# Kernel optimization log

Hardware: AMD Instinct MI355X
Metric: run time of the kernel (lower is better)

## Reference

```python
import jax, jax.numpy as jnp
import numpy as np

D = 512   # dense write dimension
M = 64    # number of experts
B = 16    # per-expert sparse code width
N = 8192  # tokens
K = 4     # experts per token (top-k)


def _normalize_U(U):
    # UnitColNormPadded(dim=1): each column of the (D+1, b) expert matrix
    # is rescaled to unit L2 norm along the padded (D+1) axis.
    nrm = jnp.sqrt(jnp.sum(U * U, axis=1, keepdims=True))
    return U / nrm


def setup_inputs() -> dict:
    key = jax.random.key(0)
    k1, k2, k3 = jax.random.split(key, 3)
    h_sparse = jax.random.normal(k1, (N, K, B), dtype=jnp.float32)
    topk_idxs = jax.random.randint(k2, (N, K), 0, M)
    U = jax.random.normal(k3, (M, D + 1, B), dtype=jnp.float32)
    return {"h_sparse": h_sparse, "topk_idxs": topk_idxs, "U": U}


def reference(h_sparse, topk_idxs, U):
    Un = _normalize_U(U)                      # (m, D+1, b)
    U_active = Un[topk_idxs][:, :, :D, :]     # gather -> (N, k, D, b)
    writes = jnp.einsum('nkdb,nkb->nd', U_active, h_sparse)   # (N, D)
    h_recon = jnp.einsum('nkdb,nd->nkb', U_active, writes)    # (N, k, b)
    h_target = jax.lax.stop_gradient(h_sparse)
    diff = h_recon - h_target
    writer_aux_loss = jnp.mean(diff * diff)
    return writes, writer_aux_loss
```

## Files before the change

kernel.cpp:

```cpp
#include <hip/hip_runtime.h>

#define DD 512
#define MM 64
#define BB 16
#define NN 8192
#define KK 4
#define DP1 513
#define CAP 1024
#define NPAIR (NN * KK)

#define CNT_B  0
#define BKT_B  33024
#define U_B    164096
#define UT_B   1212672
#define WBF_B  2261248
#define PART_B 10649856
#define WS_NEED 44204288

typedef unsigned int uint;
typedef unsigned short ushort;
typedef __attribute__((ext_vector_type(8))) short short8;
typedef __attribute__((ext_vector_type(4))) float f32x4;

__device__ __forceinline__ ushort f2bf(float f) {
    uint u = __builtin_bit_cast(uint, f);
    uint r = (u + 0x7FFFu + ((u >> 16) & 1u)) >> 16;
    return (ushort)r;
}
__device__ __forceinline__ float bf2f(ushort s) {
    return __builtin_bit_cast(float, (uint)s << 16);
}

__global__ __launch_bounds__(256) void prep_build(
    const float* __restrict__ U,
    const int*   __restrict__ topk,
    void* __restrict__ ws,
    float* __restrict__ loss_slot)
{
    const int blk = blockIdx.x, t = threadIdx.x;

    if (blk < 256) {
        const int m = blk >> 2, sl = blk & 3;
        const float* Um = U + (long)m * DP1 * BB;

        __shared__ float red[256];
        __shared__ float inv_s[BB];
        __shared__ ushort tr[BB][136];

        float a = 0.f;
        for (int i = t; i < DP1 * BB; i += 256) { float v = Um[i]; a += v * v; }
        red[t] = a;
        __syncthreads();
        if (t < BB) {
            float tot = 0.f;
            #pragma unroll
            for (int j = 0; j < 16; ++j) tot += red[t + 16 * j];
            inv_s[t] = rsqrtf(tot);
        }
        __syncthreads();

        ushort* ub = (ushort*)((char*)ws + U_B) + (long)m * DD * BB + sl * 2048;
        ushort* ut = (ushort*)((char*)ws + UT_B) + (long)m * BB * DD + sl * 128;
        const float* Us = Um + sl * 2048;

        #pragma unroll
        for (int iter = 0; iter < 4; ++iter) {
            const int i = t + iter * 256;
            const int e0 = 2 * i;
            const int dl = e0 >> 4, b0 = e0 & 15;
            const float2 v = *(const float2*)(Us + e0);
            const ushort bv0 = f2bf(v.x * inv_s[b0]);
            const ushort bv1 = f2bf(v.y * inv_s[b0 + 1]);
            *(uint*)(ub + e0) = (uint)bv0 | ((uint)bv1 << 16);
            tr[b0][dl]     = bv0;
            tr[b0 + 1][dl] = bv1;
        }
        __syncthreads();
        {
            const int b = t >> 4, doff = (t & 15) * 8;
            uint4 val;
            val.x = (uint)tr[b][doff + 0] | ((uint)tr[b][doff + 1] << 16);
            val.y = (uint)tr[b][doff + 2] | ((uint)tr[b][doff + 3] << 16);
            val.z = (uint)tr[b][doff + 4] | ((uint)tr[b][doff + 5] << 16);
            val.w = (uint)tr[b][doff + 6] | ((uint)tr[b][doff + 7] << 16);
            *(uint4*)(ut + (long)b * DD + doff) = val;
        }
    } else {
        const int cblk = blk - 256;
        int* cnt = (int*)ws;
        ushort* bkt = (ushort*)((char*)ws + BKT_B);
        __shared__ int lc[MM], lb[MM];
        if (t < MM) lc[t] = 0;
        __syncthreads();
        const int p = cblk * 256 + t;
        const int e = topk[p];
        const int my = atomicAdd(&lc[e], 1);
        __syncthreads();
        if (t < MM) lb[t] = atomicAdd(&cnt[t], lc[t]);
        __syncthreads();
        bkt[e * CAP + lb[e] + my] = (ushort)p;
        if (cblk == 0 && t == 0) *loss_slot = 0.f;
    }
}

__global__ __launch_bounds__(256) void pass_writes_mfma(
    const float* __restrict__ h_sparse, void* __restrict__ ws)
{
    const int e = blockIdx.x & 63, g = blockIdx.x >> 6;
    const int wave = threadIdx.x >> 6, lane = threadIdx.x & 63;
    const int quad = lane >> 4, l15 = lane & 15;

    const int* cnt = (const int*)ws;
    const ushort* bkt = (const ushort*)((const char*)ws + BKT_B);
    const ushort* Ue = (const ushort*)((const char*)ws + U_B) + (long)e * DD * BB;
    ushort* part = (ushort*)((char*)ws + PART_B);

    const int c  = cnt[e];
    const int lo = (c * g) >> 3;
    const int hi = (c * (g + 1)) >> 3;

    for (int base = lo + wave * 16; base < hi; base += 64) {
        const int pidx = base + l15;
        const bool valid = pidx < hi;
        const int id = valid ? (int)bkt[e * CAP + pidx] : 0;
        const int n = id >> 2, k = id & 3;

        short8 bfrag = (short8)0;
        if (quad < 2 && valid) {
            const float4* hp = (const float4*)(h_sparse + (long)id * BB + quad * 8);
            const float4 h0 = hp[0], h1 = hp[1];
            bfrag[0] = (short)f2bf(h0.x); bfrag[1] = (short)f2bf(h0.y);
            bfrag[2] = (short)f2bf(h0.z); bfrag[3] = (short)f2bf(h0.w);
            bfrag[4] = (short)f2bf(h1.x); bfrag[5] = (short)f2bf(h1.y);
            bfrag[6] = (short)f2bf(h1.z); bfrag[7] = (short)f2bf(h1.w);
        }
        ushort* prow = part + ((long)(k * NN + n) << 9);

        #pragma unroll 2
        for (int dt = 0; dt < 32; dt += 2) {
            short8 a0 = (short8)0, a1 = (short8)0;
            if (quad < 2) {
                a0 = *(const short8*)(Ue + ((long)(dt * 16 + l15) << 4) + quad * 8);
                a1 = *(const short8*)(Ue + ((long)((dt + 1) * 16 + l15) << 4) + quad * 8);
            }
            f32x4 z = {0.f, 0.f, 0.f, 0.f};
            f32x4 c0 = __builtin_amdgcn_mfma_f32_16x16x32_bf16(a0, bfrag, z, 0, 0, 0);
            f32x4 c1 = __builtin_amdgcn_mfma_f32_16x16x32_bf16(a1, bfrag, z, 0, 0, 0);

            uint p0x = (uint)f2bf(c0[0]) | ((uint)f2bf(c0[1]) << 16);
            uint p0y = (uint)f2bf(c0[2]) | ((uint)f2bf(c0[3]) << 16);
            uint p1x = (uint)f2bf(c1[0]) | ((uint)f2bf(c1[1]) << 16);
            uint p1y = (uint)f2bf(c1[2]) | ((uint)f2bf(c1[3]) << 16);
            uint q0x = __shfl_xor((int)p0x, 16, 64);
            uint q0y = __shfl_xor((int)p0y, 16, 64);
            uint q1x = __shfl_xor((int)p1x, 16, 64);
            uint q1y = __shfl_xor((int)p1y, 16, 64);

            if (valid) {
                uint4 st;
                int sdt;
                if ((quad & 1) == 0) { st.x = p0x; st.y = p0y; st.z = q0x; st.w = q0y; sdt = dt; }
                else                 { st.x = q1x; st.y = q1y; st.z = p1x; st.w = p1y; sdt = dt + 1; }
                const int srow = (quad & 2) ? 8 : 0;
                *(uint4*)(prow + sdt * 16 + srow) = st;
            }
        }
    }
}

__global__ __launch_bounds__(256) void reduce_w(
    void* __restrict__ ws, float* __restrict__ out)
{
    const uint4* part4 = (const uint4*)((const char*)ws + PART_B);
    uint4* wbf4 = (uint4*)((char*)ws + WBF_B);
    const int gsz = NN * DD / 8;
    const int gid = blockIdx.x * 256 + threadIdx.x;

    const uint4 v0 = part4[gid];
    const uint4 v1 = part4[(long)gsz + gid];
    const uint4 v2 = part4[2L * gsz + gid];
    const uint4 v3 = part4[3L * gsz + gid];

    float s[8];
    s[0] = bf2f((ushort)v0.x) + bf2f((ushort)v1.x) + bf2f((ushort)v2.x) + bf2f((ushort)v3.x);
    s[1] = bf2f((ushort)(v0.x >> 16)) + bf2f((ushort)(v1.x >> 16)) + bf2f((ushort)(v2.x >> 16)) + bf2f((ushort)(v3.x >> 16));
    s[2] = bf2f((ushort)v0.y) + bf2f((ushort)v1.y) + bf2f((ushort)v2.y) + bf2f((ushort)v3.y);
    s[3] = bf2f((ushort)(v0.y >> 16)) + bf2f((ushort)(v1.y >> 16)) + bf2f((ushort)(v2.y >> 16)) + bf2f((ushort)(v3.y >> 16));
    s[4] = bf2f((ushort)v0.z) + bf2f((ushort)v1.z) + bf2f((ushort)v2.z) + bf2f((ushort)v3.z);
    s[5] = bf2f((ushort)(v0.z >> 16)) + bf2f((ushort)(v1.z >> 16)) + bf2f((ushort)(v2.z >> 16)) + bf2f((ushort)(v3.z >> 16));
    s[6] = bf2f((ushort)v0.w) + bf2f((ushort)v1.w) + bf2f((ushort)v2.w) + bf2f((ushort)v3.w);
    s[7] = bf2f((ushort)(v0.w >> 16)) + bf2f((ushort)(v1.w >> 16)) + bf2f((ushort)(v2.w >> 16)) + bf2f((ushort)(v3.w >> 16));

    float4* out4 = (float4*)out;
    out4[(long)gid * 2 + 0] = make_float4(s[0], s[1], s[2], s[3]);
    out4[(long)gid * 2 + 1] = make_float4(s[4], s[5], s[6], s[7]);

    uint4 pk;
    pk.x = (uint)f2bf(s[0]) | ((uint)f2bf(s[1]) << 16);
    pk.y = (uint)f2bf(s[2]) | ((uint)f2bf(s[3]) << 16);
    pk.z = (uint)f2bf(s[4]) | ((uint)f2bf(s[5]) << 16);
    pk.w = (uint)f2bf(s[6]) | ((uint)f2bf(s[7]) << 16);
    wbf4[gid] = pk;
}

__global__ __launch_bounds__(256) void pass_recon_mfma(
    const float* __restrict__ h_sparse, void* __restrict__ ws,
    float* __restrict__ out)
{
    const int e = blockIdx.x & 63, g = blockIdx.x >> 6;
    const int wave = threadIdx.x >> 6, lane = threadIdx.x & 63;
    const int quad = lane >> 4, l15 = lane & 15;
    const int t = threadIdx.x;

    const int* cnt = (const int*)ws;
    const ushort* bkt = (const ushort*)((const char*)ws + BKT_B);
    const ushort* Ute = (const ushort*)((const char*)ws + UT_B) + (long)e * BB * DD;
    const ushort* wbf = (const ushort*)((const char*)ws + WBF_B);

    __shared__ float loss_blk;
    if (t == 0) loss_blk = 0.f;
    __syncthreads();

    const int c  = cnt[e];
    const int lo = (c * g) >> 3;
    const int hi = (c * (g + 1)) >> 3;

    float lsum = 0.f;
    for (int base = lo + wave * 16; base < hi; base += 64) {
        const int pidx = base + l15;
        const bool valid = pidx < hi;
        const int id = valid ? (int)bkt[e * CAP + pidx] : 0;
        const int n = id >> 2;
        const ushort* wrow = wbf + ((long)n << 9);

        f32x4 acc = {0.f, 0.f, 0.f, 0.f};
        #pragma unroll 4
        for (int kk = 0; kk < 16; ++kk) {
            const int doff = kk * 32 + quad * 8;
            const short8 afrag = *(const short8*)(wrow + doff);
            const short8 bfrag = *(const short8*)(Ute + (long)l15 * DD + doff);
            acc = __builtin_amdgcn_mfma_f32_16x16x32_bf16(afrag, bfrag, acc, 0, 0, 0);
        }
        #pragma unroll
        for (int r = 0; r < 4; ++r) {
            const int pr = base + quad * 4 + r;
            if (pr < hi) {
                const int id2 = (int)bkt[e * CAP + pr];
                const float h = h_sparse[(long)id2 * BB + l15];
                const float d = acc[r] - h;
                lsum += d * d;
            }
        }
    }
    #pragma unroll
    for (int off = 32; off > 0; off >>= 1) lsum += __shfl_xor(lsum, off, 64);
    if (lane == 0 && lsum != 0.f) atomicAdd(&loss_blk, lsum);
    __syncthreads();
    if (t == 0 && loss_blk != 0.f)
        atomicAdd(out + (long)NN * DD, loss_blk * (1.0f / ((float)NN * KK * BB)));
}

__global__ __launch_bounds__(256) void norm_kernel(
    const float* __restrict__ U, float* __restrict__ inv_norm,
    float* __restrict__ loss_slot)
{
    const int m = blockIdx.x;
    const int t = threadIdx.x;
    const float* Um = U + (long)m * DP1 * BB;
    float acc = 0.f;
    for (int idx = t; idx < DP1 * BB; idx += 256) {
        float v = Um[idx];
        acc += v * v;
    }
    __shared__ float s[256];
    s[t] = acc;
    __syncthreads();
    if (t < BB) {
        float tot = 0.f;
        #pragma unroll
        for (int j = 0; j < 16; ++j) tot += s[t + 16 * j];
        inv_norm[m * BB + t] = rsqrtf(tot);
    }
    if (m == 0 && t == 0) *loss_slot = 0.f;
}

__global__ __launch_bounds__(256) void dense_write_kernel(
    const float* __restrict__ h_sparse,
    const int*   __restrict__ topk,
    const float* __restrict__ U,
    const float* __restrict__ inv_norm,
    float* __restrict__ out)
{
    const int n = blockIdx.x;
    const int t = threadIdx.x;

    __shared__ float hs[KK * BB];
    __shared__ float ho[KK * BB];
    __shared__ float inv_s[KK * BB];
    __shared__ int   eidx[KK];
    __shared__ float w_s[DD];
    __shared__ float red[256];

    if (t < KK) eidx[t] = topk[n * KK + t];
    __syncthreads();
    if (t < KK * BB) {
        const int k = t / BB, b = t % BB;
        const float h  = h_sparse[(long)n * KK * BB + t];
        const float iv = inv_norm[eidx[k] * BB + b];
        ho[t]    = h;
        inv_s[t] = iv;
        hs[t]    = h * iv;
    }
    __syncthreads();

    #pragma unroll
    for (int dd = 0; dd < 2; ++dd) {
        const int d = t + dd * 256;
        float w = 0.f;
        #pragma unroll
        for (int k = 0; k < KK; ++k) {
            const float4* row = (const float4*)(U + ((long)eidx[k] * DP1 + d) * BB);
            #pragma unroll
            for (int q = 0; q < 4; ++q) {
                const float4 u4 = row[q];
                w += u4.x * hs[k * BB + 4 * q + 0];
                w += u4.y * hs[k * BB + 4 * q + 1];
                w += u4.z * hs[k * BB + 4 * q + 2];
                w += u4.w * hs[k * BB + 4 * q + 3];
            }
        }
        w_s[d] = w;
        out[(long)n * DD + d] = w;
    }
    __syncthreads();

    {
        const int pair = t & 63;
        const int k = pair >> 4, b = pair & 15;
        const int ch = t >> 6;
        const float* Ucol = U + (long)eidx[k] * DP1 * BB + b;
        float p = 0.f;
        #pragma unroll 8
        for (int d = ch * 128; d < ch * 128 + 128; ++d) {
            p += Ucol[(long)d * BB] * w_s[d];
        }
        red[t] = p;
    }
    __syncthreads();

    if (t < 64) {
        const float recon = (red[t] + red[t + 64] + red[t + 128] + red[t + 192]) * inv_s[t];
        const float diff  = recon - ho[t];
        float sq = diff * diff;
        #pragma unroll
        for (int off = 32; off > 0; off >>= 1) sq += __shfl_down(sq, off, 64);
        if (t == 0) {
            atomicAdd(out + (long)NN * DD, sq * (1.0f / ((float)NN * KK * BB)));
        }
    }
}


extern "C" void kernel_launch(void* const* d_in, const int* in_sizes, int n_in,
                              void* d_out, int out_size, void* d_ws, size_t ws_size,
                              hipStream_t stream) {
    const float* h_sparse = (const float*)d_in[0];
    const int*   topk     = (const int*)d_in[1];
    const float* U        = (const float*)d_in[2];
    float* out = (float*)d_out;

    if (ws_size >= (size_t)WS_NEED) {
        hipMemsetAsync(d_ws, 0, 256, stream);
        hipLaunchKernelGGL(prep_build, dim3(256 + NPAIR / 256), dim3(256), 0, stream,
                           U, topk, d_ws, out + (long)NN * DD);
        hipLaunchKernelGGL(pass_writes_mfma, dim3(MM * 8), dim3(256), 0, stream,
                           h_sparse, d_ws);
        hipLaunchKernelGGL(reduce_w, dim3(NN * DD / 8 / 256), dim3(256), 0, stream,
                           d_ws, out);
        hipLaunchKernelGGL(pass_recon_mfma, dim3(MM * 8), dim3(256), 0, stream,
                           h_sparse, d_ws, out);
    } else {
        float* inv_norm = (float*)d_ws;
        hipLaunchKernelGGL(norm_kernel, dim3(MM), dim3(256), 0, stream,
                           U, inv_norm, out + (long)NN * DD);
        hipLaunchKernelGGL(dense_write_kernel, dim3(NN), dim3(256), 0, stream,
                           h_sparse, topk, U, inv_norm, out);
    }
}
```

Measured before the change: 126.5 us.

## Accumulate writes with fp32 atomics into output instead of partials plus reduce

Removes the per-k bf16 partial buffer and the separate reduce kernel. The writes pass now atomically adds MFMA results straight into a zeroed fp32 output, and the recon pass reads fp32 writes and converts them to bf16 on the fly. This saves a 32MB partial write-and-read round trip and one launch. In exchange it issues many scalar float atomics, adds a memset of the output, and makes the summation order nondeterministic.

```diff
diff --git a/kernel.cpp b/kernel.cpp
--- a/kernel.cpp
+++ b/kernel.cpp
@@ -10,12 +10,10 @@
 #define NPAIR (NN * KK)
 
 #define CNT_B  0
-#define BKT_B  33024
-#define U_B    164096
-#define UT_B   1212672
-#define WBF_B  2261248
-#define PART_B 10649856
-#define WS_NEED 44204288
+#define BKT_B  256
+#define U_B    131328
+#define UT_B   1179904
+#define WS_NEED 2228480
 
 typedef unsigned int uint;
 typedef unsigned short ushort;
@@ -34,8 +32,7 @@
 __global__ __launch_bounds__(256) void prep_build(
     const float* __restrict__ U,
     const int*   __restrict__ topk,
-    void* __restrict__ ws,
-    float* __restrict__ loss_slot)
+    void* __restrict__ ws)
 {
     const int blk = blockIdx.x, t = threadIdx.x;
 
@@ -99,12 +96,12 @@
         if (t < MM) lb[t] = atomicAdd(&cnt[t], lc[t]);
         __syncthreads();
         bkt[e * CAP + lb[e] + my] = (ushort)p;
-        if (cblk == 0 && t == 0) *loss_slot = 0.f;
-    }
-}
-
-__global__ __launch_bounds__(256) void pass_writes_mfma(
-    const float* __restrict__ h_sparse, void* __restrict__ ws)
+    }
+}
+
+__global__ __launch_bounds__(256) void pass_writes_at(
+    const float* __restrict__ h_sparse, const void* __restrict__ ws,
+    float* __restrict__ out)
 {
     const int e = blockIdx.x & 63, g = blockIdx.x >> 6;
     const int wave = threadIdx.x >> 6, lane = threadIdx.x & 63;
@@ -113,7 +110,6 @@
     const int* cnt = (const int*)ws;
     const ushort* bkt = (const ushort*)((const char*)ws + BKT_B);
     const ushort* Ue = (const ushort*)((const char*)ws + U_B) + (long)e * DD * BB;
-    ushort* part = (ushort*)((char*)ws + PART_B);
 
     const int c  = cnt[e];
     const int lo = (c * g) >> 3;
@@ -123,7 +119,7 @@
         const int pidx = base + l15;
         const bool valid = pidx < hi;
         const int id = valid ? (int)bkt[e * CAP + pidx] : 0;
-        const int n = id >> 2, k = id & 3;
+        const int n = id >> 2;
 
         short8 bfrag = (short8)0;
         if (quad < 2 && valid) {
@@ -134,77 +130,28 @@
             bfrag[4] = (short)f2bf(h1.x); bfrag[5] = (short)f2bf(h1.y);
             bfrag[6] = (short)f2bf(h1.z); bfrag[7] = (short)f2bf(h1.w);
         }
-        ushort* prow = part + ((long)(k * NN + n) << 9);
-
-        #pragma unroll 2
-        for (int dt = 0; dt < 32; dt += 2) {
-            short8 a0 = (short8)0, a1 = (short8)0;
-            if (quad < 2) {
-                a0 = *(const short8*)(Ue + ((long)(dt * 16 + l15) << 4) + quad * 8);
-                a1 = *(const short8*)(Ue + ((long)((dt + 1) * 16 + l15) << 4) + quad * 8);
+        float* orow = out + (long)n * DD;
+
+        #pragma unroll 4
+        for (int dt = 0; dt < 32; ++dt) {
+            short8 afrag = (short8)0;
+            if (quad < 2)
+                afrag = *(const short8*)(Ue + ((long)(dt * 16 + l15) << 4) + quad * 8);
+            f32x4 z = {0.f, 0.f, 0.f, 0.f};
+            f32x4 acc = __builtin_amdgcn_mfma_f32_16x16x32_bf16(afrag, bfrag, z, 0, 0, 0);
+            if (valid) {
+                float* p = orow + dt * 16 + quad * 4;
+                atomicAdd(p + 0, acc[0]);
+                atomicAdd(p + 1, acc[1]);
+                atomicAdd(p + 2, acc[2]);
+                atomicAdd(p + 3, acc[3]);
             }
-            f32x4 z = {0.f, 0.f, 0.f, 0.f};
-            f32x4 c0 = __builtin_amdgcn_mfma_f32_16x16x32_bf16(a0, bfrag, z, 0, 0, 0);
-            f32x4 c1 = __builtin_amdgcn_mfma_f32_16x16x32_bf16(a1, bfrag, z, 0, 0, 0);
-
-            uint p0x = (uint)f2bf(c0[0]) | ((uint)f2bf(c0[1]) << 16);
-            uint p0y = (uint)f2bf(c0[2]) | ((uint)f2bf(c0[3]) << 16);
-            uint p1x = (uint)f2bf(c1[0]) | ((uint)f2bf(c1[1]) << 16);
-            uint p1y = (uint)f2bf(c1[2]) | ((uint)f2bf(c1[3]) << 16);
-            uint q0x = __shfl_xor((int)p0x, 16, 64);
-            uint q0y = __shfl_xor((int)p0y, 16, 64);
-            uint q1x = __shfl_xor((int)p1x, 16, 64);
-            uint q1y = __shfl_xor((int)p1y, 16, 64);
-
-            if (valid) {
-                uint4 st;
-                int sdt;
-                if ((quad & 1) == 0) { st.x = p0x; st.y = p0y; st.z = q0x; st.w = q0y; sdt = dt; }
-                else                 { st.x = q1x; st.y = q1y; st.z = p1x; st.w = p1y; sdt = dt + 1; }
-                const int srow = (quad & 2) ? 8 : 0;
-                *(uint4*)(prow + sdt * 16 + srow) = st;
-            }
-        }
-    }
-}
-
-__global__ __launch_bounds__(256) void reduce_w(
-    void* __restrict__ ws, float* __restrict__ out)
-{
-    const uint4* part4 = (const uint4*)((const char*)ws + PART_B);
-    uint4* wbf4 = (uint4*)((char*)ws + WBF_B);
-    const int gsz = NN * DD / 8;
-    const int gid = blockIdx.x * 256 + threadIdx.x;
-
-    const uint4 v0 = part4[gid];
-    const uint4 v1 = part4[(long)gsz + gid];
-    const uint4 v2 = part4[2L * gsz + gid];
-    const uint4 v3 = part4[3L * gsz + gid];
-
-    float s[8];
-    s[0] = bf2f((ushort)v0.x) + bf2f((ushort)v1.x) + bf2f((ushort)v2.x) + bf2f((ushort)v3.x);
-    s[1] = bf2f((ushort)(v0.x >> 16)) + bf2f((ushort)(v1.x >> 16)) + bf2f((ushort)(v2.x >> 16)) + bf2f((ushort)(v3.x >> 16));
-    s[2] = bf2f((ushort)v0.y) + bf2f((ushort)v1.y) + bf2f((ushort)v2.y) + bf2f((ushort)v3.y);
-    s[3] = bf2f((ushort)(v0.y >> 16)) + bf2f((ushort)(v1.y >> 16)) + bf2f((ushort)(v2.y >> 16)) + bf2f((ushort)(v3.y >> 16));
-    s[4] = bf2f((ushort)v0.z) + bf2f((ushort)v1.z) + bf2f((ushort)v2.z) + bf2f((ushort)v3.z);
-    s[5] = bf2f((ushort)(v0.z >> 16)) + bf2f((ushort)(v1.z >> 16)) + bf2f((ushort)(v2.z >> 16)) + bf2f((ushort)(v3.z >> 16));
-    s[6] = bf2f((ushort)v0.w) + bf2f((ushort)v1.w) + bf2f((ushort)v2.w) + bf2f((ushort)v3.w);
-    s[7] = bf2f((ushort)(v0.w >> 16)) + bf2f((ushort)(v1.w >> 16)) + bf2f((ushort)(v2.w >> 16)) + bf2f((ushort)(v3.w >> 16));
-
-    float4* out4 = (float4*)out;
-    out4[(long)gid * 2 + 0] = make_float4(s[0], s[1], s[2], s[3]);
-    out4[(long)gid * 2 + 1] = make_float4(s[4], s[5], s[6], s[7]);
-
-    uint4 pk;
-    pk.x = (uint)f2bf(s[0]) | ((uint)f2bf(s[1]) << 16);
-    pk.y = (uint)f2bf(s[2]) | ((uint)f2bf(s[3]) << 16);
-    pk.z = (uint)f2bf(s[4]) | ((uint)f2bf(s[5]) << 16);
-    pk.w = (uint)f2bf(s[6]) | ((uint)f2bf(s[7]) << 16);
-    wbf4[gid] = pk;
-}
-
-__global__ __launch_bounds__(256) void pass_recon_mfma(
-    const float* __restrict__ h_sparse, void* __restrict__ ws,
+        }
+    }
+}
+
+__global__ __launch_bounds__(256) void pass_recon_f32(
+    const float* __restrict__ h_sparse, const void* __restrict__ ws,
     float* __restrict__ out)
 {
     const int e = blockIdx.x & 63, g = blockIdx.x >> 6;
@@ -215,7 +162,6 @@
     const int* cnt = (const int*)ws;
     const ushort* bkt = (const ushort*)((const char*)ws + BKT_B);
     const ushort* Ute = (const ushort*)((const char*)ws + UT_B) + (long)e * BB * DD;
-    const ushort* wbf = (const ushort*)((const char*)ws + WBF_B);
 
     __shared__ float loss_blk;
     if (t == 0) loss_blk = 0.f;
@@ -231,13 +177,19 @@
         const bool valid = pidx < hi;
         const int id = valid ? (int)bkt[e * CAP + pidx] : 0;
         const int n = id >> 2;
-        const ushort* wrow = wbf + ((long)n << 9);
+        const float* wrow = out + (long)n * DD;
 
         f32x4 acc = {0.f, 0.f, 0.f, 0.f};
         #pragma unroll 4
         for (int kk = 0; kk < 16; ++kk) {
             const int doff = kk * 32 + quad * 8;
-            const short8 afrag = *(const short8*)(wrow + doff);
+            const float4 f0 = *(const float4*)(wrow + doff);
+            const float4 f1 = *(const float4*)(wrow + doff + 4);
+            short8 afrag;
+            afrag[0] = (short)f2bf(f0.x); afrag[1] = (short)f2bf(f0.y);
+            afrag[2] = (short)f2bf(f0.z); afrag[3] = (short)f2bf(f0.w);
+            afrag[4] = (short)f2bf(f1.x); afrag[5] = (short)f2bf(f1.y);
+            afrag[6] = (short)f2bf(f1.z); afrag[7] = (short)f2bf(f1.w);
             const short8 bfrag = *(const short8*)(Ute + (long)l15 * DD + doff);
             acc = __builtin_amdgcn_mfma_f32_16x16x32_bf16(afrag, bfrag, acc, 0, 0, 0);
         }
@@ -371,13 +323,12 @@
 
     if (ws_size >= (size_t)WS_NEED) {
         hipMemsetAsync(d_ws, 0, 256, stream);
+        hipMemsetAsync(d_out, 0, ((size_t)NN * DD + 1) * 4, stream);
         hipLaunchKernelGGL(prep_build, dim3(256 + NPAIR / 256), dim3(256), 0, stream,
-                           U, topk, d_ws, out + (long)NN * DD);
-        hipLaunchKernelGGL(pass_writes_mfma, dim3(MM * 8), dim3(256), 0, stream,
-                           h_sparse, d_ws);
-        hipLaunchKernelGGL(reduce_w, dim3(NN * DD / 8 / 256), dim3(256), 0, stream,
-                           d_ws, out);
-        hipLaunchKernelGGL(pass_recon_mfma, dim3(MM * 8), dim3(256), 0, stream,
+                           U, topk, d_ws);
+        hipLaunchKernelGGL(pass_writes_at, dim3(MM * 8), dim3(256), 0, stream,
+                           h_sparse, d_ws, out);
+        hipLaunchKernelGGL(pass_recon_f32, dim3(MM * 8), dim3(256), 0, stream,
                            h_sparse, d_ws, out);
     } else {
         float* inv_norm = (float*)d_ws;
```

Result: slower. 347.8 us (+174.9%).

## Compute reconstruction loss via expert Gram matrices instead of re-reading writes

Applied to the files above, without the earlier changes.

Replaces the per-pair reconstruction pass (which re-read bf16 writes through a gather) with a precomputed 64x64 table of 16x16 expert Gram blocks U_e^T U_e'. The loss is then evaluated per token from h_sparse and the Gram blocks. The Gram computation is folded into the writes kernel's grid, and the loss is folded into the reduce kernel's grid. This removes one launch and the bf16 writes buffer round trip, at the cost of an extra 4 MB Gram table and somewhat different rounding, since the Gram path uses bf16 U and fp32 h.

```diff
diff --git a/kernel.cpp b/kernel.cpp
--- a/kernel.cpp
+++ b/kernel.cpp
@@ -10,12 +10,12 @@
 #define NPAIR (NN * KK)
 
 #define CNT_B  0
-#define BKT_B  33024
-#define U_B    164096
-#define UT_B   1212672
-#define WBF_B  2261248
-#define PART_B 10649856
-#define WS_NEED 44204288
+#define BKT_B  256
+#define U_B    131328
+#define UT_B   1179904
+#define G_B    2228480
+#define PART_B 6422784
+#define WS_NEED 39977216
 
 typedef unsigned int uint;
 typedef unsigned short ushort;
@@ -103,161 +103,158 @@
     }
 }
 
-__global__ __launch_bounds__(256) void pass_writes_mfma(
+__global__ __launch_bounds__(256) void writes_gram(
     const float* __restrict__ h_sparse, void* __restrict__ ws)
 {
-    const int e = blockIdx.x & 63, g = blockIdx.x >> 6;
-    const int wave = threadIdx.x >> 6, lane = threadIdx.x & 63;
+    const int blk = blockIdx.x, t = threadIdx.x;
+    const int wave = t >> 6, lane = t & 63;
     const int quad = lane >> 4, l15 = lane & 15;
 
-    const int* cnt = (const int*)ws;
-    const ushort* bkt = (const ushort*)((const char*)ws + BKT_B);
-    const ushort* Ue = (const ushort*)((const char*)ws + U_B) + (long)e * DD * BB;
-    ushort* part = (ushort*)((char*)ws + PART_B);
-
-    const int c  = cnt[e];
-    const int lo = (c * g) >> 3;
-    const int hi = (c * (g + 1)) >> 3;
-
-    for (int base = lo + wave * 16; base < hi; base += 64) {
-        const int pidx = base + l15;
-        const bool valid = pidx < hi;
-        const int id = valid ? (int)bkt[e * CAP + pidx] : 0;
-        const int n = id >> 2, k = id & 3;
-
-        short8 bfrag = (short8)0;
-        if (quad < 2 && valid) {
-            const float4* hp = (const float4*)(h_sparse + (long)id * BB + quad * 8);
-            const float4 h0 = hp[0], h1 = hp[1];
-            bfrag[0] = (short)f2bf(h0.x); bfrag[1] = (short)f2bf(h0.y);
-            bfrag[2] = (short)f2bf(h0.z); bfrag[3] = (short)f2bf(h0.w);
-            bfrag[4] = (short)f2bf(h1.x); bfrag[5] = (short)f2bf(h1.y);
-            bfrag[6] = (short)f2bf(h1.z); bfrag[7] = (short)f2bf(h1.w);
-        }
-        ushort* prow = part + ((long)(k * NN + n) << 9);
-
-        #pragma unroll 2
-        for (int dt = 0; dt < 32; dt += 2) {
-            short8 a0 = (short8)0, a1 = (short8)0;
-            if (quad < 2) {
-                a0 = *(const short8*)(Ue + ((long)(dt * 16 + l15) << 4) + quad * 8);
-                a1 = *(const short8*)(Ue + ((long)((dt + 1) * 16 + l15) << 4) + quad * 8);
+    if (blk < 512) {
+        const int e = blk & 63, g = blk >> 6;
+        const int* cnt = (const int*)ws;
+        const ushort* bkt = (const ushort*)((const char*)ws + BKT_B);
+        const ushort* Ue = (const ushort*)((const char*)ws + U_B) + (long)e * DD * BB;
+        ushort* part = (ushort*)((char*)ws + PART_B);
+
+        const int c  = cnt[e];
+        const int lo = (c * g) >> 3;
+        const int hi = (c * (g + 1)) >> 3;
+
+        for (int base = lo + wave * 16; base < hi; base += 64) {
+            const int pidx = base + l15;
+            const bool valid = pidx < hi;
+            const int id = valid ? (int)bkt[e * CAP + pidx] : 0;
+            const int n = id >> 2, k = id & 3;
+
+            short8 bfrag = (short8)0;
+            if (quad < 2 && valid) {
+                const float4* hp = (const float4*)(h_sparse + (long)id * BB + quad * 8);
+                const float4 h0 = hp[0], h1 = hp[1];
+                bfrag[0] = (short)f2bf(h0.x); bfrag[1] = (short)f2bf(h0.y);
+                bfrag[2] = (short)f2bf(h0.z); bfrag[3] = (short)f2bf(h0.w);
+                bfrag[4] = (short)f2bf(h1.x); bfrag[5] = (short)f2bf(h1.y);
+                bfrag[6] = (short)f2bf(h1.z); bfrag[7] = (short)f2bf(h1.w);
             }
-            f32x4 z = {0.f, 0.f, 0.f, 0.f};
-            f32x4 c0 = __builtin_amdgcn_mfma_f32_16x16x32_bf16(a0, bfrag, z, 0, 0, 0);
-            f32x4 c1 = __builtin_amdgcn_mfma_f32_16x16x32_bf16(a1, bfrag, z, 0, 0, 0);
-
-            uint p0x = (uint)f2bf(c0[0]) | ((uint)f2bf(c0[1]) << 16);
-            uint p0y = (uint)f2bf(c0[2]) | ((uint)f2bf(c0[3]) << 16);
-            uint p1x = (uint)f2bf(c1[0]) | ((uint)f2bf(c1[1]) << 16);
-            uint p1y = (uint)f2bf(c1[2]) | ((uint)f2bf(c1[3]) << 16);
-            uint q0x = __shfl_xor((int)p0x, 16, 64);
-            uint q0y = __shfl_xor((int)p0y, 16, 64);
-            uint q1x = __shfl_xor((int)p1x, 16, 64);
-            uint q1y = __shfl_xor((int)p1y, 16, 64);
-
-            if (valid) {
-                uint4 st;
-                int sdt;
-                if ((quad & 1) == 0) { st.x = p0x; st.y = p0y; st.z = q0x; st.w = q0y; sdt = dt; }
-                else                 { st.x = q1x; st.y = q1y; st.z = p1x; st.w = p1y; sdt = dt + 1; }
-                const int srow = (quad & 2) ? 8 : 0;
-                *(uint4*)(prow + sdt * 16 + srow) = st;
+            ushort* prow = part + ((long)(k * NN + n) << 9);
+
+            #pragma unroll 2
+            for (int dt = 0; dt < 32; dt += 2) {
+                short8 a0 = (short8)0, a1 = (short8)0;
+                if (quad < 2) {
+                    a0 = *(const short8*)(Ue + ((long)(dt * 16 + l15) << 4) + quad * 8);
+                    a1 = *(const short8*)(Ue + ((long)((dt + 1) * 16 + l15) << 4) + quad * 8);
+                }
+                f32x4 z = {0.f, 0.f, 0.f, 0.f};
+                f32x4 c0 = __builtin_amdgcn_mfma_f32_16x16x32_bf16(a0, bfrag, z, 0, 0, 0);
+                f32x4 c1 = __builtin_amdgcn_mfma_f32_16x16x32_bf16(a1, bfrag, z, 0, 0, 0);
+
+                uint p0x = (uint)f2bf(c0[0]) | ((uint)f2bf(c0[1]) << 16);
+                uint p0y = (uint)f2bf(c0[2]) | ((uint)f2bf(c0[3]) << 16);
+                uint p1x = (uint)f2bf(c1[0]) | ((uint)f2bf(c1[1]) << 16);
+                uint p1y = (uint)f2bf(c1[2]) | ((uint)f2bf(c1[3]) << 16);
+                uint q0x = __shfl_xor((int)p0x, 16, 64);
+                uint q0y = __shfl_xor((int)p0y, 16, 64);
+                uint q1x = __shfl_xor((int)p1x, 16, 64);
+                uint q1y = __shfl_xor((int)p1y, 16, 64);
+
+                if (valid) {
+                    uint4 st;
+                    int sdt;
+                    if ((quad & 1) == 0) { st.x = p0x; st.y = p0y; st.z = q0x; st.w = q0y; sdt = dt; }
+                    else                 { st.x = q1x; st.y = q1y; st.z = p1x; st.w = p1y; sdt = dt + 1; }
+                    const int srow = (quad & 2) ? 8 : 0;
+                    *(uint4*)(prow + sdt * 16 + srow) = st;
+                }
             }
         }
-    }
-}
-
-__global__ __launch_bounds__(256) void reduce_w(
-    void* __restrict__ ws, float* __restrict__ out)
-{
-    const uint4* part4 = (const uint4*)((const char*)ws + PART_B);
-    uint4* wbf4 = (uint4*)((char*)ws + WBF_B);
-    const int gsz = NN * DD / 8;
-    const int gid = blockIdx.x * 256 + threadIdx.x;
-
-    const uint4 v0 = part4[gid];
-    const uint4 v1 = part4[(long)gsz + gid];
-    const uint4 v2 = part4[2L * gsz + gid];
-    const uint4 v3 = part4[3L * gsz + gid];
-
-    float s[8];
-    s[0] = bf2f((ushort)v0.x) + bf2f((ushort)v1.x) + bf2f((ushort)v2.x) + bf2f((ushort)v3.x);
-    s[1] = bf2f((ushort)(v0.x >> 16)) + bf2f((ushort)(v1.x >> 16)) + bf2f((ushort)(v2.x >> 16)) + bf2f((ushort)(v3.x >> 16));
-    s[2] = bf2f((ushort)v0.y) + bf2f((ushort)v1.y) + bf2f((ushort)v2.y) + bf2f((ushort)v3.y);
-    s[3] = bf2f((ushort)(v0.y >> 16)) + bf2f((ushort)(v1.y >> 16)) + bf2f((ushort)(v2.y >> 16)) + bf2f((ushort)(v3.y >> 16));
-    s[4] = bf2f((ushort)v0.z) + bf2f((ushort)v1.z) + bf2f((ushort)v2.z) + bf2f((ushort)v3.z);
-    s[5] = bf2f((ushort)(v0.z >> 16)) + bf2f((ushort)(v1.z >> 16)) + bf2f((ushort)(v2.z >> 16)) + bf2f((ushort)(v3.z >> 16));
-    s[6] = bf2f((ushort)v0.w) + bf2f((ushort)v1.w) + bf2f((ushort)v2.w) + bf2f((ushort)v3.w);
-    s[7] = bf2f((ushort)(v0.w >> 16)) + bf2f((ushort)(v1.w >> 16)) + bf2f((ushort)(v2.w >> 16)) + bf2f((ushort)(v3.w >> 16));
-
-    float4* out4 = (float4*)out;
-    out4[(long)gid * 2 + 0] = make_float4(s[0], s[1], s[2], s[3]);
-    out4[(long)gid * 2 + 1] = make_float4(s[4], s[5], s[6], s[7]);
-
-    uint4 pk;
-    pk.x = (uint)f2bf(s[0]) | ((uint)f2bf(s[1]) << 16);
-    pk.y = (uint)f2bf(s[2]) | ((uint)f2bf(s[3]) << 16);
-    pk.z = (uint)f2bf(s[4]) | ((uint)f2bf(s[5]) << 16);
-    pk.w = (uint)f2bf(s[6]) | ((uint)f2bf(s[7]) << 16);
-    wbf4[gid] = pk;
-}
-
-__global__ __launch_bounds__(256) void pass_recon_mfma(
-    const float* __restrict__ h_sparse, void* __restrict__ ws,
-    float* __restrict__ out)
-{
-    const int e = blockIdx.x & 63, g = blockIdx.x >> 6;
-    const int wave = threadIdx.x >> 6, lane = threadIdx.x & 63;
-    const int quad = lane >> 4, l15 = lane & 15;
-    const int t = threadIdx.x;
-
-    const int* cnt = (const int*)ws;
-    const ushort* bkt = (const ushort*)((const char*)ws + BKT_B);
-    const ushort* Ute = (const ushort*)((const char*)ws + UT_B) + (long)e * BB * DD;
-    const ushort* wbf = (const ushort*)((const char*)ws + WBF_B);
-
-    __shared__ float loss_blk;
-    if (t == 0) loss_blk = 0.f;
-    __syncthreads();
-
-    const int c  = cnt[e];
-    const int lo = (c * g) >> 3;
-    const int hi = (c * (g + 1)) >> 3;
-
-    float lsum = 0.f;
-    for (int base = lo + wave * 16; base < hi; base += 64) {
-        const int pidx = base + l15;
-        const bool valid = pidx < hi;
-        const int id = valid ? (int)bkt[e * CAP + pidx] : 0;
-        const int n = id >> 2;
-        const ushort* wrow = wbf + ((long)n << 9);
+    } else {
+        const int p = (blk - 512) * 4 + wave;
+        const int e1 = p >> 6, e2 = p & 63;
+        const ushort* utb = (const ushort*)((const char*)ws + UT_B);
+        const ushort* Ut1 = utb + (long)e1 * BB * DD;
+        const ushort* Ut2 = utb + (long)e2 * BB * DD;
+        float* G = (float*)((char*)ws + G_B);
 
         f32x4 acc = {0.f, 0.f, 0.f, 0.f};
         #pragma unroll 4
         for (int kk = 0; kk < 16; ++kk) {
             const int doff = kk * 32 + quad * 8;
-            const short8 afrag = *(const short8*)(wrow + doff);
-            const short8 bfrag = *(const short8*)(Ute + (long)l15 * DD + doff);
+            const short8 afrag = *(const short8*)(Ut1 + (long)l15 * DD + doff);
+            const short8 bfrag = *(const short8*)(Ut2 + (long)l15 * DD + doff);
             acc = __builtin_amdgcn_mfma_f32_16x16x32_bf16(afrag, bfrag, acc, 0, 0, 0);
         }
-        #pragma unroll
-        for (int r = 0; r < 4; ++r) {
-            const int pr = base + quad * 4 + r;
-            if (pr < hi) {
-                const int id2 = (int)bkt[e * CAP + pr];
-                const float h = h_sparse[(long)id2 * BB + l15];
-                const float d = acc[r] - h;
-                lsum += d * d;
-            }
-        }
-    }
-    #pragma unroll
-    for (int off = 32; off > 0; off >>= 1) lsum += __shfl_xor(lsum, off, 64);
-    if (lane == 0 && lsum != 0.f) atomicAdd(&loss_blk, lsum);
-    __syncthreads();
-    if (t == 0 && loss_blk != 0.f)
-        atomicAdd(out + (long)NN * DD, loss_blk * (1.0f / ((float)NN * KK * BB)));
+        float* gbase = G + (((long)e1 * 64 + e2) << 8);
+        *(float4*)(gbase + l15 * 16 + quad * 4) = *(float4*)&acc;
+    }
+}
+
+__global__ __launch_bounds__(256) void reduce_loss(
+    const float* __restrict__ h_sparse,
+    const int*   __restrict__ topk,
+    const void* __restrict__ ws,
+    float* __restrict__ out)
+{
+    const int blk = blockIdx.x, t = threadIdx.x;
+
+    if (blk < 2048) {
+        const uint4* part4 = (const uint4*)((const char*)ws + PART_B);
+        const int gsz = NN * DD / 8;
+        const int gid = blk * 256 + t;
+
+        const uint4 v0 = part4[gid];
+        const uint4 v1 = part4[(long)gsz + gid];
+        const uint4 v2 = part4[2L * gsz + gid];
+        const uint4 v3 = part4[3L * gsz + gid];
+
+        float s[8];
+        s[0] = bf2f((ushort)v0.x) + bf2f((ushort)v1.x) + bf2f((ushort)v2.x) + bf2f((ushort)v3.x);
+        s[1] = bf2f((ushort)(v0.x >> 16)) + bf2f((ushort)(v1.x >> 16)) + bf2f((ushort)(v2.x >> 16)) + bf2f((ushort)(v3.x >> 16));
+        s[2] = bf2f((ushort)v0.y) + bf2f((ushort)v1.y) + bf2f((ushort)v2.y) + bf2f((ushort)v3.y);
+        s[3] = bf2f((ushort)(v0.y >> 16)) + bf2f((ushort)(v1.y >> 16)) + bf2f((ushort)(v2.y >> 16)) + bf2f((ushort)(v3.y >> 16));
+        s[4] = bf2f((ushort)v0.z) + bf2f((ushort)v1.z) + bf2f((ushort)v2.z) + bf2f((ushort)v3.z);
+        s[5] = bf2f((ushort)(v0.z >> 16)) + bf2f((ushort)(v1.z >> 16)) + bf2f((ushort)(v2.z >> 16)) + bf2f((ushort)(v3.z >> 16));
+        s[6] = bf2f((ushort)v0.w) + bf2f((ushort)v1.w) + bf2f((ushort)v2.w) + bf2f((ushort)v3.w);
+        s[7] = bf2f((ushort)(v0.w >> 16)) + bf2f((ushort)(v1.w >> 16)) + bf2f((ushort)(v2.w >> 16)) + bf2f((ushort)(v3.w >> 16));
+
+        float4* out4 = (float4*)out;
+        out4[(long)gid * 2 + 0] = make_float4(s[0], s[1], s[2], s[3]);
+        out4[(long)gid * 2 + 1] = make_float4(s[4], s[5], s[6], s[7]);
+    } else {
+        const int wave = t >> 6, lane = t & 63;
+        const int k = lane >> 4, b = lane & 15;
+        const int tok = (blk - 2048) * 4 + wave;
+        const float* G = (const float*)((const char*)ws + G_B);
+
+        __shared__ float s_h[4][64];
+        __shared__ int   s_e[4][4];
+        __shared__ float s_loss[4];
+
+        s_h[wave][lane] = h_sparse[(long)tok * 64 + lane];
+        if (lane < 4) s_e[wave][lane] = topk[tok * 4 + lane];
+        __syncthreads();
+
+        const int ek = s_e[wave][k];
+        float r = 0.f;
+        #pragma unroll
+        for (int kp = 0; kp < 4; ++kp) {
+            const float* grow = G + (((long)ek * 64 + s_e[wave][kp]) << 8) + b;
+            const float* hp = &s_h[wave][kp * 16];
+            #pragma unroll
+            for (int bp = 0; bp < 16; ++bp)
+                r += grow[bp * 16] * hp[bp];
+        }
+        const float d = r - s_h[wave][lane];
+        float lsum = d * d;
+        #pragma unroll
+        for (int off = 32; off > 0; off >>= 1) lsum += __shfl_xor(lsum, off, 64);
+        if (lane == 0) s_loss[wave] = lsum;
+        __syncthreads();
+        if (t == 0) {
+            const float tot = s_loss[0] + s_loss[1] + s_loss[2] + s_loss[3];
+            atomicAdd(out + (long)NN * DD, tot * (1.0f / ((float)NN * KK * BB)));
+        }
+    }
 }
 
 __global__ __launch_bounds__(256) void norm_kernel(
@@ -373,12 +370,10 @@
         hipMemsetAsync(d_ws, 0, 256, stream);
         hipLaunchKernelGGL(prep_build, dim3(256 + NPAIR / 256), dim3(256), 0, stream,
                            U, topk, d_ws, out + (long)NN * DD);
-        hipLaunchKernelGGL(pass_writes_mfma, dim3(MM * 8), dim3(256), 0, stream,
+        hipLaunchKernelGGL(writes_gram, dim3(512 + 1024), dim3(256), 0, stream,
                            h_sparse, d_ws);
-        hipLaunchKernelGGL(reduce_w, dim3(NN * DD / 8 / 256), dim3(256), 0, stream,
-                           d_ws, out);
-        hipLaunchKernelGGL(pass_recon_mfma, dim3(MM * 8), dim3(256), 0, stream,
-                           h_sparse, d_ws, out);
+        hipLaunchKernelGGL(reduce_loss, dim3(2048 + 2048), dim3(256), 0, stream,
+                           h_sparse, topk, d_ws, out);
     } else {
         float* inv_norm = (float*)d_ws;
         hipLaunchKernelGGL(norm_kernel, dim3(MM), dim3(256), 0, stream,
```

Measured after the change: 140.8 us. 1.11x slower.

## Split each expert's work over 32 groups and the D dimension across waves

Applied to the files above, without the earlier changes.

Raises the grid from 8 to 32 blocks per expert. Inside each block, the four waves now share one 16-pair tile and split the D dimension among themselves, where before each wave took its own pair tiles. In the recon pass the per-wave partial dot products are summed through shared memory with two barriers per tile, and wave 0 alone computes the loss and does a single atomic. The workspace offsets are also compacted because the count area shrinks. The aim is to fill more CUs and spread the uneven per-expert load. The cost is block-level syncs and waves 1-3 sitting idle during the loss step.

```diff
diff --git a/kernel.cpp b/kernel.cpp
--- a/kernel.cpp
+++ b/kernel.cpp
@@ -7,15 +7,16 @@
 #define KK 4
 #define DP1 513
 #define CAP 1024
+#define GPE 32
 #define NPAIR (NN * KK)
 
 #define CNT_B  0
-#define BKT_B  33024
-#define U_B    164096
-#define UT_B   1212672
-#define WBF_B  2261248
-#define PART_B 10649856
-#define WS_NEED 44204288
+#define BKT_B  256
+#define U_B    131328
+#define UT_B   1179904
+#define WBF_B  2228224
+#define PART_B 10616832
+#define WS_NEED 44171264
 
 typedef unsigned int uint;
 typedef unsigned short ushort;
@@ -116,10 +117,11 @@
     ushort* part = (ushort*)((char*)ws + PART_B);
 
     const int c  = cnt[e];
-    const int lo = (c * g) >> 3;
-    const int hi = (c * (g + 1)) >> 3;
-
-    for (int base = lo + wave * 16; base < hi; base += 64) {
+    const int lo = (c * g) >> 5;
+    const int hi = (c * (g + 1)) >> 5;
+    const int dt0 = wave * 8;
+
+    for (int base = lo; base < hi; base += 16) {
         const int pidx = base + l15;
         const bool valid = pidx < hi;
         const int id = valid ? (int)bkt[e * CAP + pidx] : 0;
@@ -136,8 +138,9 @@
         }
         ushort* prow = part + ((long)(k * NN + n) << 9);
 
-        #pragma unroll 2
-        for (int dt = 0; dt < 32; dt += 2) {
+        #pragma unroll
+        for (int j = 0; j < 4; ++j) {
+            const int dt = dt0 + 2 * j;
             short8 a0 = (short8)0, a1 = (short8)0;
             if (quad < 2) {
                 a0 = *(const short8*)(Ue + ((long)(dt * 16 + l15) << 4) + quad * 8);
@@ -210,23 +213,21 @@
     const int e = blockIdx.x & 63, g = blockIdx.x >> 6;
     const int wave = threadIdx.x >> 6, lane = threadIdx.x & 63;
     const int quad = lane >> 4, l15 = lane & 15;
-    const int t = threadIdx.x;
 
     const int* cnt = (const int*)ws;
     const ushort* bkt = (const ushort*)((const char*)ws + BKT_B);
     const ushort* Ute = (const ushort*)((const char*)ws + UT_B) + (long)e * BB * DD;
     const ushort* wbf = (const ushort*)((const char*)ws + WBF_B);
 
-    __shared__ float loss_blk;
-    if (t == 0) loss_blk = 0.f;
-    __syncthreads();
+    __shared__ float s_part[4][64][4];
 
     const int c  = cnt[e];
-    const int lo = (c * g) >> 3;
-    const int hi = (c * (g + 1)) >> 3;
+    const int lo = (c * g) >> 5;
+    const int hi = (c * (g + 1)) >> 5;
 
     float lsum = 0.f;
-    for (int base = lo + wave * 16; base < hi; base += 64) {
+
+    for (int base = lo; base < hi; base += 16) {
         const int pidx = base + l15;
         const bool valid = pidx < hi;
         const int id = valid ? (int)bkt[e * CAP + pidx] : 0;
@@ -234,30 +235,46 @@
         const ushort* wrow = wbf + ((long)n << 9);
 
         f32x4 acc = {0.f, 0.f, 0.f, 0.f};
-        #pragma unroll 4
-        for (int kk = 0; kk < 16; ++kk) {
-            const int doff = kk * 32 + quad * 8;
+        #pragma unroll
+        for (int j = 0; j < 4; ++j) {
+            const int doff = (wave * 4 + j) * 32 + quad * 8;
             const short8 afrag = *(const short8*)(wrow + doff);
             const short8 bfrag = *(const short8*)(Ute + (long)l15 * DD + doff);
             acc = __builtin_amdgcn_mfma_f32_16x16x32_bf16(afrag, bfrag, acc, 0, 0, 0);
         }
-        #pragma unroll
-        for (int r = 0; r < 4; ++r) {
-            const int pr = base + quad * 4 + r;
-            if (pr < hi) {
-                const int id2 = (int)bkt[e * CAP + pr];
-                const float h = h_sparse[(long)id2 * BB + l15];
-                const float d = acc[r] - h;
-                lsum += d * d;
+        *(float4*)&s_part[wave][lane][0] = *(float4*)&acc;
+        __syncthreads();
+
+        if (wave == 0) {
+            const float4 p0 = *(const float4*)&s_part[0][lane][0];
+            const float4 p1 = *(const float4*)&s_part[1][lane][0];
+            const float4 p2 = *(const float4*)&s_part[2][lane][0];
+            const float4 p3 = *(const float4*)&s_part[3][lane][0];
+            float tot[4];
+            tot[0] = p0.x + p1.x + p2.x + p3.x;
+            tot[1] = p0.y + p1.y + p2.y + p3.y;
+            tot[2] = p0.z + p1.z + p2.z + p3.z;
+            tot[3] = p0.w + p1.w + p2.w + p3.w;
+            #pragma unroll
+            for (int r = 0; r < 4; ++r) {
+                const int pr = base + quad * 4 + r;
+                if (pr < hi) {
+                    const int id2 = (int)bkt[e * CAP + pr];
+                    const float h = h_sparse[(long)id2 * BB + l15];
+                    const float d = tot[r] - h;
+                    lsum += d * d;
+                }
             }
         }
-    }
-    #pragma unroll
-    for (int off = 32; off > 0; off >>= 1) lsum += __shfl_xor(lsum, off, 64);
-    if (lane == 0 && lsum != 0.f) atomicAdd(&loss_blk, lsum);
-    __syncthreads();
-    if (t == 0 && loss_blk != 0.f)
-        atomicAdd(out + (long)NN * DD, loss_blk * (1.0f / ((float)NN * KK * BB)));
+        __syncthreads();
+    }
+
+    if (wave == 0) {
+        #pragma unroll
+        for (int off = 32; off > 0; off >>= 1) lsum += __shfl_xor(lsum, off, 64);
+        if (lane == 0 && lsum != 0.f)
+            atomicAdd(out + (long)NN * DD, lsum * (1.0f / ((float)NN * KK * BB)));
+    }
 }
 
 __global__ __launch_bounds__(256) void norm_kernel(
@@ -373,11 +390,11 @@
         hipMemsetAsync(d_ws, 0, 256, stream);
         hipLaunchKernelGGL(prep_build, dim3(256 + NPAIR / 256), dim3(256), 0, stream,
                            U, topk, d_ws, out + (long)NN * DD);
-        hipLaunchKernelGGL(pass_writes_mfma, dim3(MM * 8), dim3(256), 0, stream,
+        hipLaunchKernelGGL(pass_writes_mfma, dim3(MM * GPE), dim3(256), 0, stream,
                            h_sparse, d_ws);
         hipLaunchKernelGGL(reduce_w, dim3(NN * DD / 8 / 256), dim3(256), 0, stream,
                            d_ws, out);
-        hipLaunchKernelGGL(pass_recon_mfma, dim3(MM * 8), dim3(256), 0, stream,
+        hipLaunchKernelGGL(pass_recon_mfma, dim3(MM * GPE), dim3(256), 0, stream,
                            h_sparse, d_ws, out);
     } else {
         float* inv_norm = (float*)d_ws;
```

After: 141.7 us. 12.0% more time.
